# Kernel tuning notes

Hardware: AMD Instinct MI355X
Metric: run time of the kernel (lower is better)

## Reference

```python
import jax, jax.numpy as jnp
import numpy as np

B, C, Ci, H, W = 64, 2048, 1024, 32, 16
BN_EPS = 1e-5

def setup_inputs() -> dict:
    key = jax.random.key(0)
    ks = jax.random.split(key, 6)
    s_in = 0.02  # small init scale for 1x1 conv weights
    return {
        "x": jax.random.normal(ks[0], (B, C, H, W), dtype=jnp.float32),
        "Wg": jax.random.normal(ks[1], (Ci, C), dtype=jnp.float32) * s_in,
        "bg": jnp.zeros((Ci,), dtype=jnp.float32),
        "Wt": jax.random.normal(ks[2], (Ci, C), dtype=jnp.float32) * s_in,
        "bt": jnp.zeros((Ci,), dtype=jnp.float32),
        "Wp": jax.random.normal(ks[3], (Ci, C), dtype=jnp.float32) * s_in,
        "bp": jnp.zeros((Ci,), dtype=jnp.float32),
        "Wo": jax.random.normal(ks[4], (C, Ci), dtype=jnp.float32) * s_in,
        "bo": jnp.zeros((C,), dtype=jnp.float32),
        "gamma": jnp.ones((C,), dtype=jnp.float32),
        "beta": jnp.zeros((C,), dtype=jnp.float32),
    }

def reference(x, Wg, bg, Wt, bt, Wp, bp, Wo, bo, gamma, beta):
    b, c, h, w = x.shape
    n = h * w
    xf = x.reshape(b, c, n)  # flatten spatial: [B, C, N]
    # 1x1 conv projections == channel GEMMs
    g  = jnp.einsum('oc,bcn->bon', Wg, xf) + bg[:, None]   # [B, Ci, N]
    th = jnp.einsum('oc,bcn->bon', Wt, xf) + bt[:, None]   # [B, Ci, N]
    ph = jnp.einsum('oc,bcn->bon', Wp, xf) + bp[:, None]   # [B, Ci, N]
    # f = theta^T @ phi : [B, N, N]
    f = jnp.einsum('bcn,bcm->bnm', th, ph)
    attn = jax.nn.softmax(f, axis=-1)
    # y = attn @ g^T, back to channels-first [B, Ci, N]
    y = jnp.einsum('bnm,bcm->bcn', attn, g)
    # output 1x1 conv + BatchNorm2d (training mode: batch stats over B and N)
    wy = jnp.einsum('oc,bcn->bon', Wo, y) + bo[:, None]    # [B, C, N]
    mean = wy.mean(axis=(0, 2), keepdims=True)
    var = wy.var(axis=(0, 2), keepdims=True)
    wy = (wy - mean) * jax.lax.rsqrt(var + BN_EPS) * gamma[:, None] + beta[:, None]
    return wy.reshape(b, c, h, w) + x
```

## Files before the change

kernel.cpp:

```cpp
#include <hip/hip_runtime.h>
#include <stdint.h>

typedef uint16_t u16;
typedef uint32_t u32;
typedef __attribute__((ext_vector_type(8))) short short8;
typedef __attribute__((ext_vector_type(4))) float f32x4;

constexpr int B_  = 64;
constexpr int C_  = 2048;
constexpr int CI_ = 1024;
constexpr int N_  = 512;
constexpr int CHB = 32;

__device__ __forceinline__ float bf2f(u16 h){
  union{u32 u; float f;} v; v.u = ((u32)h) << 16; return v.f;
}
__device__ __forceinline__ u16 f2bf(float x){
  union{float f; u32 u;} v; v.f = x;
  u32 u = v.u;
  u32 r = u + 0x7fffu + ((u >> 16) & 1u);
  return (u16)(r >> 16);
}
__device__ __forceinline__ u32 split2(float v){
  u16 hi = f2bf(v);
  u16 lo = f2bf(v - bf2f(hi));
  return (u32)hi | ((u32)lo << 16);
}

__device__ __forceinline__ void gld_lds16(const void* gsrc, void* ldst){
  __builtin_amdgcn_global_load_lds(
      (__attribute__((address_space(1))) void*)(const_cast<void*>(gsrc)),
      (__attribute__((address_space(3))) void*)(ldst), 16, 0, 0);
}

template<int TM, int TN, int BIAS_MODE, int OUT_MODE, bool BSPLIT>
__global__ __launch_bounds__(512, 2)
void gemm_nt_p4(const u16* __restrict__ A, long aBatch, int lda,
                const u16* __restrict__ Bm, long bBatch, int ldb,
                void* __restrict__ Out, long oBatch, int ldo,
                const float* __restrict__ bias, int K)
{
  constexpr int BK   = 32;
  constexpr int WM   = TM / 2;
  constexpr int WN   = TN / 4;
  constexpr int AFR  = WM / 16;
  constexpr int BFR  = WN / 16;
  constexpr int SLOT = (TM + TN) * BK;
  constexpr int SOPS = (TM + TN) / 128;
  __shared__ __align__(16) u16 sm[4 * SLOT];

  const int bz = blockIdx.z;
  const int tm = blockIdx.x * TM;
  const int tn = blockIdx.y * TN;
  const u16* Ab = A  + (long)bz * aBatch;
  const u16* Bb = Bm + (long)bz * bBatch;

  const int tid  = threadIdx.x;
  const int wave = tid >> 6;
  const int lane = tid & 63;
  const int wr   = wave >> 2;
  const int wc   = wave & 3;
  const int lrow = lane & 15;
  const int quad = lane >> 4;

  const int NT = K / BK;

  f32x4 acc[AFR][BFR];
#pragma unroll
  for (int i = 0; i < AFR; ++i)
#pragma unroll
    for (int j = 0; j < BFR; ++j) acc[i][j] = f32x4{0.f, 0.f, 0.f, 0.f};

  short8 afA[AFR], afB[AFR], bfr[BFR];

#define STAGE(kt) do{ \
    u16* sl = &sm[((kt) & 3) * SLOT]; \
    const long kof = (long)(kt) * BK; \
    _Pragma("unroll") \
    for (int r = 0; r < TM / 128; ++r){ \
      const int c   = tid + 512 * r; \
      const int row = c >> 2; \
      const int sc  = ((c & 3) ^ ((row >> 1) & 3)) << 3; \
      gld_lds16(Ab + (long)(tm + row) * lda + kof + sc, sl + c * 8); \
    } \
    _Pragma("unroll") \
    for (int r = 0; r < TN / 128; ++r){ \
      const int c   = tid + 512 * r; \
      const int row = c >> 2; \
      const int sc  = ((c & 3) ^ ((row >> 1) & 3)) << 3; \
      gld_lds16(Bb + (long)(tn + row) * ldb + kof + sc, sl + TM * BK + c * 8); \
    } \
  }while(0)

#define LOADAF(tt, DST) do{ \
    const u16* Asl = &sm[((tt) & 3) * SLOT]; \
    _Pragma("unroll") \
    for (int i = 0; i < AFR; ++i){ \
      const int r8 = i * 16 + lrow; \
      DST[i] = *(const short8*)&Asl[(wr * WM + r8) * BK + ((quad ^ ((r8 >> 1) & 3)) << 3)]; \
    } \
  }while(0)

#define LOADBF(tt) do{ \
    const u16* Bsl = &sm[((tt) & 3) * SLOT + TM * BK]; \
    _Pragma("unroll") \
    for (int j = 0; j < BFR; ++j){ \
      const int n8 = j * 16 + lrow; \
      bfr[j] = *(const short8*)&Bsl[(wc * WN + n8) * BK + ((quad ^ ((n8 >> 1) & 3)) << 3)]; \
    } \
  }while(0)

#define MFMA_CL(AF) do{ \
    __builtin_amdgcn_s_setprio(1); \
    _Pragma("unroll") \
    for (int j = 0; j < BFR; ++j){ \
      const short8 b0 = bfr[j]; \
      const short8 b1 = __builtin_shufflevector(b0, b0, 1, 0, 3, 2, 5, 4, 7, 6); \
      _Pragma("unroll") \
      for (int i = 0; i < AFR; ++i){ \
        acc[i][j] = __builtin_amdgcn_mfma_f32_16x16x32_bf16(AF[i], b0, acc[i][j], 0, 0, 0); \
        if (BSPLIT) \
          acc[i][j] = __builtin_amdgcn_mfma_f32_16x16x32_bf16(AF[i], b1, acc[i][j], 0, 0, 0); \
      } \
    } \
    __builtin_amdgcn_s_setprio(0); \
  }while(0)

#define BAR() do{ asm volatile("" ::: "memory"); __builtin_amdgcn_s_barrier(); \
                  asm volatile("" ::: "memory"); }while(0)
#define VMW2() do{ if constexpr (SOPS == 4) asm volatile("s_waitcnt vmcnt(8)" ::: "memory"); \
                   else                      asm volatile("s_waitcnt vmcnt(6)" ::: "memory"); }while(0)
#define VMW1() do{ if constexpr (SOPS == 4) asm volatile("s_waitcnt vmcnt(4)" ::: "memory"); \
                   else                      asm volatile("s_waitcnt vmcnt(3)" ::: "memory"); }while(0)
#define VMW0() asm volatile("s_waitcnt vmcnt(0)" ::: "memory")

  STAGE(0); STAGE(1); STAGE(2);
  VMW2(); BAR();
  LOADAF(0, afA);

  int t = 0;
  for (; t + 4 < NT; t += 2){
    STAGE(t + 3); VMW2(); BAR(); LOADBF(t);     LOADAF(t + 1, afB); MFMA_CL(afA); BAR();
    STAGE(t + 4); VMW2(); BAR(); LOADBF(t + 1); LOADAF(t + 2, afA); MFMA_CL(afB); BAR();
  }
  STAGE(NT - 1); VMW2(); BAR(); LOADBF(NT - 4); LOADAF(NT - 3, afB); MFMA_CL(afA); BAR();
  VMW1();        BAR(); LOADBF(NT - 3); LOADAF(NT - 2, afA); MFMA_CL(afB); BAR();
  VMW0();        BAR(); LOADBF(NT - 2); LOADAF(NT - 1, afB); MFMA_CL(afA); BAR();
  LOADBF(NT - 1); MFMA_CL(afB);

#undef STAGE
#undef LOADAF
#undef LOADBF
#undef MFMA_CL
#undef BAR
#undef VMW2
#undef VMW1
#undef VMW0

  const long obase = (long)bz * oBatch;
#pragma unroll
  for (int i = 0; i < AFR; ++i){
    const int rbase = tm + wr * WM + i * 16 + quad * 4;
#pragma unroll
    for (int j = 0; j < BFR; ++j){
      const int col = tn + wc * WN + j * 16 + lrow;
      float cb = 0.f;
      if (BIAS_MODE == 2) cb = bias[col];
#pragma unroll
      for (int r = 0; r < 4; ++r){
        const int row = rbase + r;
        float v = acc[i][j][r];
        if (BIAS_MODE == 1) v += bias[row];
        if (BIAS_MODE == 2) v += cb;
        if (OUT_MODE == 1){
          ((float*)Out)[obase + (long)row * ldo + col] = v;
        } else if (OUT_MODE == 0){
          ((u16*)Out)[obase + (long)row * ldo + col] = f2bf(v);
        } else {
          *(u32*)((u16*)Out + obase + (long)row * ldo + col * 2) = split2(v);
        }
      }
    }
  }
}

__global__ __launch_bounds__(1024)
void transpose_split_k(const float* __restrict__ x, u32* __restrict__ xT2)
{
  __shared__ float t[32][33];
  const int b  = blockIdx.z;
  const int n0 = blockIdx.x << 5;
  const int c0 = blockIdx.y << 5;
  const float* xb = x + (long)b * ((long)C_ * N_);
  u32* xo = xT2 + (long)b * ((long)N_ * C_);
  t[threadIdx.y][threadIdx.x] = xb[(long)(c0 + threadIdx.y) * N_ + n0 + threadIdx.x];
  __syncthreads();
  xo[(long)(n0 + threadIdx.y) * C_ + c0 + threadIdx.x] = split2(t[threadIdx.x][threadIdx.y]);
}

__global__ __launch_bounds__(256)
void wsplit_k(const float* __restrict__ W, u32* __restrict__ W2)
{
  const long i = ((long)blockIdx.x * 256 + threadIdx.x) * 4;
  const float4 v = *(const float4*)(W + i);
  uint4 o;
  o.x = split2(v.x); o.y = split2(v.y); o.z = split2(v.z); o.w = split2(v.w);
  *(uint4*)(W2 + i) = o;
}

__global__ __launch_bounds__(256)
void pack_bf16_k(const float* __restrict__ W, u16* __restrict__ Wb)
{
  const long i = ((long)blockIdx.x * 256 + threadIdx.x) * 8;
  const float4 a = *(const float4*)(W + i);
  const float4 b = *(const float4*)(W + i + 4);
  uint4 o;
  o.x = (u32)f2bf(a.x) | ((u32)f2bf(a.y) << 16);
  o.y = (u32)f2bf(a.z) | ((u32)f2bf(a.w) << 16);
  o.z = (u32)f2bf(b.x) | ((u32)f2bf(b.y) << 16);
  o.w = (u32)f2bf(b.z) | ((u32)f2bf(b.w) << 16);
  *(uint4*)(Wb + i) = o;
}

__global__ __launch_bounds__(256)
void softmax_k(float* __restrict__ f)
{
  const long row = blockIdx.x;
  float* fr = f + (row << 9);
  const int tid = threadIdx.x;
  const float v0 = fr[tid];
  const float v1 = fr[tid + 256];

  float m = fmaxf(v0, v1);
#pragma unroll
  for (int off = 32; off; off >>= 1) m = fmaxf(m, __shfl_xor(m, off, 64));
  __shared__ float red[8];
  const int wave = tid >> 6, lane = tid & 63;
  if (!lane) red[wave] = m;
  __syncthreads();
  m = fmaxf(fmaxf(red[0], red[1]), fmaxf(red[2], red[3]));

  const float e0 = __expf(v0 - m);
  const float e1 = __expf(v1 - m);
  float s = e0 + e1;
#pragma unroll
  for (int off = 32; off; off >>= 1) s += __shfl_xor(s, off, 64);
  if (!lane) red[4 + wave] = s;
  __syncthreads();
  const float rs = 1.f / (red[4] + red[5] + red[6] + red[7]);

  u16* ar = (u16*)fr;
  ar[tid]       = f2bf(e0 * rs);
  ar[tid + 256] = f2bf(e1 * rs);
}

__global__ __launch_bounds__(256)
void bn_stats_k(const u16* __restrict__ wy, float* __restrict__ stats)
{
  const int c = blockIdx.x;
  const int tid = threadIdx.x;
  float s = 0.f, q = 0.f;
  const u16* base = wy + (long)c * N_;
  for (int b = 0; b < B_; ++b){
    const u32 w = ((const u32*)(base + (long)b * ((long)C_ * N_)))[tid];
    const float a0 = bf2f((u16)(w & 0xffff));
    const float a1 = bf2f((u16)(w >> 16));
    s += a0 + a1;
    q += a0 * a0 + a1 * a1;
  }
#pragma unroll
  for (int off = 32; off; off >>= 1){ s += __shfl_xor(s, off, 64); q += __shfl_xor(q, off, 64); }
  __shared__ float rs_[4], rq_[4];
  const int wave = tid >> 6, lane = tid & 63;
  if (!lane){ rs_[wave] = s; rq_[wave] = q; }
  __syncthreads();
  if (tid == 0){
    const float S = rs_[0] + rs_[1] + rs_[2] + rs_[3];
    const float Q = rq_[0] + rq_[1] + rq_[2] + rq_[3];
    const float inv = 1.f / (float)(B_ * N_);
    const float mean = S * inv;
    const float var  = Q * inv - mean * mean;
    stats[c]      = mean;
    stats[C_ + c] = rsqrtf(var + 1e-5f);
  }
}

__global__ __launch_bounds__(256)
void bn_apply_k(const u16* __restrict__ wy, const float* __restrict__ x,
                const float* __restrict__ stats,
                const float* __restrict__ gamma, const float* __restrict__ beta,
                float* __restrict__ out)
{
  const long i = ((long)blockIdx.x * 256 + threadIdx.x) * 8;
  const int c = (int)((i >> 9) & (C_ - 1));
  const float a  = stats[C_ + c] * gamma[c];
  const float b0 = beta[c] - stats[c] * a;

  const uint4 wv = *(const uint4*)(wy + i);
  const float4 x0 = *(const float4*)(x + i);
  const float4 x1 = *(const float4*)(x + i + 4);
  float4 o0, o1;
  o0.x = bf2f((u16)(wv.x & 0xffff)) * a + b0 + x0.x;
  o0.y = bf2f((u16)(wv.x >> 16))    * a + b0 + x0.y;
  o0.z = bf2f((u16)(wv.y & 0xffff)) * a + b0 + x0.z;
  o0.w = bf2f((u16)(wv.y >> 16))    * a + b0 + x0.w;
  o1.x = bf2f((u16)(wv.z & 0xffff)) * a + b0 + x1.x;
  o1.y = bf2f((u16)(wv.z >> 16))    * a + b0 + x1.y;
  o1.z = bf2f((u16)(wv.w & 0xffff)) * a + b0 + x1.z;
  o1.w = bf2f((u16)(wv.w >> 16))    * a + b0 + x1.w;
  *(float4*)(out + i)     = o0;
  *(float4*)(out + i + 4) = o1;
}

extern "C" void kernel_launch(void* const* d_in, const int* in_sizes, int n_in,
                              void* d_out, int out_size, void* d_ws, size_t ws_size,
                              hipStream_t stream)
{
  (void)in_sizes; (void)n_in; (void)out_size; (void)ws_size;
  const float* x     = (const float*)d_in[0];
  const float* Wg    = (const float*)d_in[1];
  const float* bg    = (const float*)d_in[2];
  const float* Wt    = (const float*)d_in[3];
  const float* bt    = (const float*)d_in[4];
  const float* Wp    = (const float*)d_in[5];
  const float* bp    = (const float*)d_in[6];
  const float* Wo    = (const float*)d_in[7];
  const float* bo    = (const float*)d_in[8];
  const float* gamma = (const float*)d_in[9];
  const float* beta  = (const float*)d_in[10];
  float* out = (float*)d_out;

  char* ob = (char*)d_out;
  u16* xT2 = (u16*)ob;
  u16* th2 = (u16*)(ob + 134217728L);
  u16* ph2 = (u16*)(ob + 134217728L + 67108864L);

  char* ws = (char*)d_ws;
  u16*   wy  = (u16*)ws;
  u16*   g   = (u16*)(ws + 134217728L);
  float* f   = (float*)(ws + 134217728L + 33554432L);
  u16*   yT  = (u16*)(ws + 134217728L + 2*33554432L);
  u32*   Wg2 = (u32*)(ws + 134217728L + 3*33554432L);
  u32*   Wt2 = Wg2 + 2097152L;
  u32*   Wp2 = Wt2 + 2097152L;
  u16*   Wob = (u16*)(Wp2 + 2097152L);
  float* stats = (float*)(Wob + 2097152L);

  wsplit_k<<<dim3(2097152 / (256 * 4)), 256, 0, stream>>>(Wg, Wg2);
  wsplit_k<<<dim3(2097152 / (256 * 4)), 256, 0, stream>>>(Wt, Wt2);
  wsplit_k<<<dim3(2097152 / (256 * 4)), 256, 0, stream>>>(Wp, Wp2);
  pack_bf16_k<<<dim3(2097152 / (256 * 8)), 256, 0, stream>>>(Wo, Wob);

  const long xBatch   = (long)C_ * N_;
  const long xt2B     = (long)N_ * 2 * C_;
  const long th2B     = (long)N_ * 2 * CI_;
  const long gB       = (long)CI_ * N_;
  const long fB       = (long)N_ * N_;
  const long attnB    = (long)N_ * 1024;
  const long yB       = (long)N_ * CI_;
  const long wyB      = (long)C_ * N_;

  for (int h = 0; h < 2; ++h){
    const float* xc = x + (long)h * CHB * xBatch;

    transpose_split_k<<<dim3(N_ / 32, C_ / 32, CHB), dim3(32, 32), 0, stream>>>(
        xc, (u32*)xT2);

    gemm_nt_p4<256, 256, 2, 2, true><<<dim3(N_ / 256, CI_ / 256, CHB), 512, 0, stream>>>(
        xT2, xt2B, 2 * C_, (const u16*)Wt2, 0L, 2 * C_, th2, th2B, 2 * CI_, bt, 2 * C_);

    gemm_nt_p4<256, 256, 2, 2, true><<<dim3(N_ / 256, CI_ / 256, CHB), 512, 0, stream>>>(
        xT2, xt2B, 2 * C_, (const u16*)Wp2, 0L, 2 * C_, ph2, th2B, 2 * CI_, bp, 2 * C_);

    gemm_nt_p4<256, 256, 1, 0, true><<<dim3(CI_ / 256, N_ / 256, CHB), 512, 0, stream>>>(
        (const u16*)Wg2, 0L, 2 * C_, xT2, xt2B, 2 * C_, g, gB, N_, bg, 2 * C_);

    gemm_nt_p4<128, 256, 0, 1, true><<<dim3(N_ / 128, N_ / 256, CHB), 512, 0, stream>>>(
        th2, th2B, 2 * CI_, ph2, th2B, 2 * CI_, f, fB, N_, nullptr, 2 * CI_);

    softmax_k<<<dim3(CHB * N_), 256, 0, stream>>>(f);

    gemm_nt_p4<256, 256, 0, 0, false><<<dim3(N_ / 256, CI_ / 256, CHB), 512, 0, stream>>>(
        (const u16*)f, attnB, 1024, g, gB, N_, yT, yB, CI_, nullptr, N_);

    gemm_nt_p4<256, 256, 1, 0, false><<<dim3(C_ / 256, N_ / 256, CHB), 512, 0, stream>>>(
        Wob, 0L, CI_, yT, yB, CI_, wy + (long)h * CHB * wyB, wyB, N_, bo, CI_);
  }

  bn_stats_k<<<dim3(C_), 256, 0, stream>>>(wy, stats);

  bn_apply_k<<<dim3((int)(((long)B_ * C_ * N_) / (256 * 8))), 256, 0, stream>>>(
      wy, x, stats, gamma, beta, out);
}
```

Before: 2.293 ms.

## Remap workgroup IDs for XCD-aware L2 locality and interleave B-fragment loads with MFMAs

Adds a workgroup ID remap that groups blocks per XCD (lid&7 round-robin), with per-GEMM ordering modes chosen so blocks that share a weight tile or batch operand land on the same XCD's L2. It also fuses the separate B-fragment LDS load and MFMA loops into one cluster that loads each B fragment just before its MFMAs, and moves the A-fragment prefetch after the MFMAs. This is meant to cut L2 misses and register pressure from holding all B fragments at once. The remap assumes the total block count is divisible by 8, and the reorder may expose LDS latency to the MFMAs.

New measurement: 2.135 ms. -6.9%, faster.

```diff
diff --git a/kernel.cpp b/kernel.cpp
--- a/kernel.cpp
+++ b/kernel.cpp
@@ -33,7 +33,7 @@
       (__attribute__((address_space(3))) void*)(ldst), 16, 0, 0);
 }
 
-template<int TM, int TN, int BIAS_MODE, int OUT_MODE, bool BSPLIT>
+template<int TM, int TN, int MODE, int BIAS_MODE, int OUT_MODE, bool BSPLIT>
 __global__ __launch_bounds__(512, 2)
 void gemm_nt_p4(const u16* __restrict__ A, long aBatch, int lda,
                 const u16* __restrict__ Bm, long bBatch, int ldb,
@@ -49,9 +49,21 @@
   constexpr int SOPS = (TM + TN) / 128;
   __shared__ __align__(16) u16 sm[4 * SLOT];
 
-  const int bz = blockIdx.z;
-  const int tm = blockIdx.x * TM;
-  const int tn = blockIdx.y * TN;
+  const int gx = gridDim.x, gy = gridDim.y, gz = gridDim.z;
+  const int nwg = gx * gy * gz;
+  const int lid = blockIdx.x + gx * (blockIdx.y + gy * blockIdx.z);
+  const int w   = (lid & 7) * (nwg >> 3) + (lid >> 3);
+  int bx, by, bz;
+  if (MODE == 0){
+    by = w % gy; const int r = w / gy; bz = r % gz; bx = r / gz;
+  } else if (MODE == 1){
+    bx = w % gx; const int r = w / gx; bz = r % gz; by = r / gz;
+  } else {
+    const int xy = w % (gx * gy); bx = xy % gx; by = xy / gx; bz = w / (gx * gy);
+  }
+
+  const int tm = bx * TM;
+  const int tn = by * TN;
   const u16* Ab = A  + (long)bz * aBatch;
   const u16* Bb = Bm + (long)bz * bBatch;
 
@@ -71,7 +83,7 @@
 #pragma unroll
     for (int j = 0; j < BFR; ++j) acc[i][j] = f32x4{0.f, 0.f, 0.f, 0.f};
 
-  short8 afA[AFR], afB[AFR], bfr[BFR];
+  short8 afA[AFR], afB[AFR];
 
 #define STAGE(kt) do{ \
     u16* sl = &sm[((kt) & 3) * SLOT]; \
@@ -101,25 +113,20 @@
     } \
   }while(0)
 
-#define LOADBF(tt) do{ \
+#define CLUST(tt, AF) do{ \
     const u16* Bsl = &sm[((tt) & 3) * SLOT + TM * BK]; \
+    __builtin_amdgcn_s_setprio(1); \
     _Pragma("unroll") \
     for (int j = 0; j < BFR; ++j){ \
       const int n8 = j * 16 + lrow; \
-      bfr[j] = *(const short8*)&Bsl[(wc * WN + n8) * BK + ((quad ^ ((n8 >> 1) & 3)) << 3)]; \
-    } \
-  }while(0)
-
-#define MFMA_CL(AF) do{ \
-    __builtin_amdgcn_s_setprio(1); \
-    _Pragma("unroll") \
-    for (int j = 0; j < BFR; ++j){ \
-      const short8 b0 = bfr[j]; \
-      const short8 b1 = __builtin_shufflevector(b0, b0, 1, 0, 3, 2, 5, 4, 7, 6); \
+      const short8 b0 = *(const short8*)&Bsl[(wc * WN + n8) * BK + ((quad ^ ((n8 >> 1) & 3)) << 3)]; \
       _Pragma("unroll") \
-      for (int i = 0; i < AFR; ++i){ \
+      for (int i = 0; i < AFR; ++i) \
         acc[i][j] = __builtin_amdgcn_mfma_f32_16x16x32_bf16(AF[i], b0, acc[i][j], 0, 0, 0); \
-        if (BSPLIT) \
+      if (BSPLIT){ \
+        const short8 b1 = __builtin_shufflevector(b0, b0, 1, 0, 3, 2, 5, 4, 7, 6); \
+        _Pragma("unroll") \
+        for (int i = 0; i < AFR; ++i) \
           acc[i][j] = __builtin_amdgcn_mfma_f32_16x16x32_bf16(AF[i], b1, acc[i][j], 0, 0, 0); \
       } \
     } \
@@ -140,18 +147,17 @@
 
   int t = 0;
   for (; t + 4 < NT; t += 2){
-    STAGE(t + 3); VMW2(); BAR(); LOADBF(t);     LOADAF(t + 1, afB); MFMA_CL(afA); BAR();
-    STAGE(t + 4); VMW2(); BAR(); LOADBF(t + 1); LOADAF(t + 2, afA); MFMA_CL(afB); BAR();
-  }
-  STAGE(NT - 1); VMW2(); BAR(); LOADBF(NT - 4); LOADAF(NT - 3, afB); MFMA_CL(afA); BAR();
-  VMW1();        BAR(); LOADBF(NT - 3); LOADAF(NT - 2, afA); MFMA_CL(afB); BAR();
-  VMW0();        BAR(); LOADBF(NT - 2); LOADAF(NT - 1, afB); MFMA_CL(afA); BAR();
-  LOADBF(NT - 1); MFMA_CL(afB);
+    STAGE(t + 3); VMW2(); BAR(); CLUST(t,     afA); LOADAF(t + 1, afB); BAR();
+    STAGE(t + 4); VMW2(); BAR(); CLUST(t + 1, afB); LOADAF(t + 2, afA); BAR();
+  }
+  STAGE(NT - 1); VMW2(); BAR(); CLUST(NT - 4, afA); LOADAF(NT - 3, afB); BAR();
+  VMW1(); BAR(); CLUST(NT - 3, afB); LOADAF(NT - 2, afA); BAR();
+  VMW0(); BAR(); CLUST(NT - 2, afA); LOADAF(NT - 1, afB); BAR();
+  CLUST(NT - 1, afB);
 
 #undef STAGE
 #undef LOADAF
-#undef LOADBF
-#undef MFMA_CL
+#undef CLUST
 #undef BAR
 #undef VMW2
 #undef VMW1
@@ -366,24 +372,24 @@
     transpose_split_k<<<dim3(N_ / 32, C_ / 32, CHB), dim3(32, 32), 0, stream>>>(
         xc, (u32*)xT2);
 
-    gemm_nt_p4<256, 256, 2, 2, true><<<dim3(N_ / 256, CI_ / 256, CHB), 512, 0, stream>>>(
+    gemm_nt_p4<256, 256, 0, 2, 2, true><<<dim3(N_ / 256, CI_ / 256, CHB), 512, 0, stream>>>(
         xT2, xt2B, 2 * C_, (const u16*)Wt2, 0L, 2 * C_, th2, th2B, 2 * CI_, bt, 2 * C_);
 
-    gemm_nt_p4<256, 256, 2, 2, true><<<dim3(N_ / 256, CI_ / 256, CHB), 512, 0, stream>>>(
+    gemm_nt_p4<256, 256, 0, 2, 2, true><<<dim3(N_ / 256, CI_ / 256, CHB), 512, 0, stream>>>(
         xT2, xt2B, 2 * C_, (const u16*)Wp2, 0L, 2 * C_, ph2, th2B, 2 * CI_, bp, 2 * C_);
 
-    gemm_nt_p4<256, 256, 1, 0, true><<<dim3(CI_ / 256, N_ / 256, CHB), 512, 0, stream>>>(
+    gemm_nt_p4<256, 256, 1, 1, 0, true><<<dim3(CI_ / 256, N_ / 256, CHB), 512, 0, stream>>>(
         (const u16*)Wg2, 0L, 2 * C_, xT2, xt2B, 2 * C_, g, gB, N_, bg, 2 * C_);
 
-    gemm_nt_p4<128, 256, 0, 1, true><<<dim3(N_ / 128, N_ / 256, CHB), 512, 0, stream>>>(
+    gemm_nt_p4<128, 256, 2, 0, 1, true><<<dim3(N_ / 128, N_ / 256, CHB), 512, 0, stream>>>(
         th2, th2B, 2 * CI_, ph2, th2B, 2 * CI_, f, fB, N_, nullptr, 2 * CI_);
 
     softmax_k<<<dim3(CHB * N_), 256, 0, stream>>>(f);
 
-    gemm_nt_p4<256, 256, 0, 0, false><<<dim3(N_ / 256, CI_ / 256, CHB), 512, 0, stream>>>(
+    gemm_nt_p4<256, 256, 2, 0, 0, false><<<dim3(N_ / 256, CI_ / 256, CHB), 512, 0, stream>>>(
         (const u16*)f, attnB, 1024, g, gB, N_, yT, yB, CI_, nullptr, N_);
 
-    gemm_nt_p4<256, 256, 1, 0, false><<<dim3(C_ / 256, N_ / 256, CHB), 512, 0, stream>>>(
+    gemm_nt_p4<256, 256, 1, 1, 0, false><<<dim3(C_ / 256, N_ / 256, CHB), 512, 0, stream>>>(
         Wob, 0L, CI_, yT, yB, CI_, wy + (long)h * CHB * wyB, wyB, N_, bo, CI_);
   }
 
```
